# Kernel tuning notes

Measured on AMD Instinct MI355X. Metric: run time of the kernel, lower is better.

Reference implementation:

```python
import jax, jax.numpy as jnp
import numpy as np

N_NODES = 50000
N_EDGES = 800000
D_IN = 512
D_HID = 64
D_OUT = 40


def setup_inputs() -> dict:
    key = jax.random.key(0)
    ks = jax.random.split(key, 8)
    x = jax.random.normal(ks[0], (N_NODES, D_IN), dtype=jnp.float32)
    edge_index = jax.random.randint(ks[1], (2, N_EDGES), 0, N_NODES, dtype=jnp.int32)
    w_mul = jax.random.uniform(ks[2], (N_EDGES,), dtype=jnp.float32)
    s1 = 1.0 / np.sqrt(D_IN)
    s2 = 1.0 / np.sqrt(D_HID)
    W1 = jax.random.uniform(ks[3], (D_IN, D_HID), minval=-s1, maxval=s1, dtype=jnp.float32)
    b1 = jax.random.uniform(ks[4], (D_HID,), minval=-s1, maxval=s1, dtype=jnp.float32)
    W2 = jax.random.uniform(ks[5], (D_HID, D_OUT), minval=-s2, maxval=s2, dtype=jnp.float32)
    b2 = jax.random.uniform(ks[6], (D_OUT,), minval=-s2, maxval=s2, dtype=jnp.float32)
    return {"x": x, "edge_index": edge_index, "w_mul": w_mul,
            "W1": W1, "b1": b1, "W2": W2, "b2": b2}


def _conv(h, src, dst, w_mul, W, b, n_nodes):
    # linear transform, then gather-scale-scatter-add (PyG aggr='add')
    h = h @ W + b                      # [N, d_out]
    msg = w_mul[:, None] * h[src]      # [E, d_out] gather + scale
    return jax.ops.segment_sum(msg, dst, num_segments=n_nodes)  # scatter-add


def reference(x, edge_index, w_mul, W1, b1, W2, b2):
    n_nodes = x.shape[0]
    src, dst = edge_index[0], edge_index[1]  # flow: source_to_target
    h = _conv(x, src, dst, w_mul, W1, b1, n_nodes)
    h = jax.nn.relu(h)
    h = _conv(h, src, dst, w_mul, W2, b2, n_nodes)
    return jax.nn.log_softmax(h, axis=1)
```

## Files before the change

### kernel.cpp

```cpp
#include <hip/hip_runtime.h>
#include <math.h>

#define D_IN  512
#define D_HID 64
#define D_OUT 40
#define CAP   64

typedef __attribute__((ext_vector_type(8))) short bf16x8;
typedef __attribute__((ext_vector_type(4))) float f32x4;

static __device__ __forceinline__ unsigned short f2bf(float f) {
    unsigned u = __float_as_uint(f);
    return (unsigned short)((u + 0x7FFF + ((u >> 16) & 1)) >> 16);
}
static __device__ __forceinline__ float bf2f(unsigned short h) {
    return __uint_as_float(((unsigned)h) << 16);
}

__global__ __launch_bounds__(256)
void prep_all(int* __restrict__ cursor, const float* __restrict__ W1,
              unsigned short* __restrict__ w1T, const float* __restrict__ W2,
              unsigned short* __restrict__ w2T, int N) {
    const int i = blockIdx.x * blockDim.x + threadIdx.x;
    if (i < N) cursor[i] = 0;
    const int j = i - N;
    if (j >= 0 && j < D_IN * D_HID) {
        const int k = j >> 6, col = j & 63;
        w1T[col * D_IN + k] = f2bf(W1[j]);
    }
    const int l = j - D_IN * D_HID;
    if (l >= 0 && l < 48 * D_HID) {
        const int col = l >> 6, k = l & 63;
        w2T[l] = (col < D_OUT) ? f2bf(W2[k * D_OUT + col]) : 0;
    }
}

__global__ __launch_bounds__(256)
void scatter_cap(const int* __restrict__ src, const int* __restrict__ dstA,
                 const float* __restrict__ wm, int* __restrict__ cursor,
                 unsigned* __restrict__ edges, int E, int N) {
    const int slice = (N + 7) >> 3;
    const int lo = (blockIdx.x & 7) * slice;
    const int hi = min(N, lo + slice);
    const int nChunk = gridDim.x >> 3;
    const int per = (E + nChunk - 1) / nChunk;
    const int beg = (blockIdx.x >> 3) * per;
    const int end = min(E, beg + per);
    for (int e = beg + threadIdx.x; e < end; e += blockDim.x) {
        const int d = dstA[e];
        if (d >= lo && d < hi) {
            const int pos = atomicAdd(&cursor[d], 1);
            if (pos < CAP)
                edges[(size_t)d * CAP + pos] =
                    ((unsigned)src[e] << 16) | (unsigned)f2bf(wm[e]);
        }
    }
}

__global__ __launch_bounds__(256)
void gemm1_mfma(const float* __restrict__ x, const unsigned short* __restrict__ w1T,
                const float* __restrict__ b1, unsigned short* __restrict__ h1, int N) {
    __shared__ unsigned char lds[8192];
    const int t = threadIdx.x;
    const int lane = t & 63;
    const int wv = t >> 6;
    const int nodeBase = blockIdx.x * 64;
    const int fr = lane & 15;
    const int fc = lane >> 4;

    int gn = nodeBase + wv * 16 + fr; if (gn >= N) gn = N - 1;
    const float* xrow = x + (size_t)gn * D_IN + fc * 8;

    f32x4 acc[4];
#pragma unroll
    for (int cg = 0; cg < 4; ++cg) acc[cg] = (f32x4){0.f, 0.f, 0.f, 0.f};

    for (int k0 = 0; k0 < D_IN; k0 += 64) {
        __syncthreads();
#pragma unroll
        for (int hh = 0; hh < 2; ++hh) {
            const int g = t + hh * 256;
            const int col = g >> 3, slot = g & 7;
            const uint4 p = *reinterpret_cast<const uint4*>(
                w1T + (size_t)col * D_IN + k0 + slot * 8);
            *reinterpret_cast<uint4*>(
                lds + col * 128 + ((slot << 4) ^ ((col & 7) << 4))) = p;
        }
        __syncthreads();

#pragma unroll
        for (int s = 0; s < 2; ++s) {
            const float4 a = *reinterpret_cast<const float4*>(xrow + k0 + s * 32);
            const float4 b = *reinterpret_cast<const float4*>(xrow + k0 + s * 32 + 4);
            uint4 p;
            p.x = (unsigned)f2bf(a.x) | ((unsigned)f2bf(a.y) << 16);
            p.y = (unsigned)f2bf(a.z) | ((unsigned)f2bf(a.w) << 16);
            p.z = (unsigned)f2bf(b.x) | ((unsigned)f2bf(b.y) << 16);
            p.w = (unsigned)f2bf(b.z) | ((unsigned)f2bf(b.w) << 16);
            const bf16x8 afrag = *reinterpret_cast<const bf16x8*>(&p);
            const int slot = s * 4 + fc;
#pragma unroll
            for (int cg = 0; cg < 4; ++cg) {
                const int brow = cg * 16 + fr;
                const bf16x8 bfrag = *reinterpret_cast<const bf16x8*>(
                    lds + brow * 128 + ((slot << 4) ^ ((brow & 7) << 4)));
                acc[cg] = __builtin_amdgcn_mfma_f32_16x16x32_bf16(afrag, bfrag, acc[cg], 0, 0, 0);
            }
        }
    }

    const int rq = lane >> 4;
#pragma unroll
    for (int cg = 0; cg < 4; ++cg) {
        const int col = cg * 16 + fr;
        const float bb = b1[col];
#pragma unroll
        for (int r = 0; r < 4; ++r) {
            const int node = nodeBase + wv * 16 + rq * 4 + r;
            if (node < N)
                h1[(size_t)node * D_HID + col] = f2bf(acc[cg][r] + bb);
        }
    }
}

__global__ __launch_bounds__(256)
void agg_hid(const unsigned short* __restrict__ h, const unsigned* __restrict__ edges,
             const int* __restrict__ count, unsigned short* __restrict__ agg1, int N) {
    const int lane = threadIdx.x & 63;
    const int n = (blockIdx.x * blockDim.x + threadIdx.x) >> 6;
    if (n >= N) return;
    const unsigned er = edges[(size_t)n * CAP + lane];
    const int cnt = min(count[n], CAP);
    float acc = 0.f;
    int j = 0;
    for (; j + 8 <= cnt; j += 8) {
        unsigned p[8];
#pragma unroll
        for (int u = 0; u < 8; ++u) p[u] = (unsigned)__shfl((int)er, j + u);
        float v[8];
#pragma unroll
        for (int u = 0; u < 8; ++u) v[u] = bf2f(h[(size_t)(p[u] >> 16) * D_HID + lane]);
#pragma unroll
        for (int u = 0; u < 8; ++u)
            acc += bf2f((unsigned short)(p[u] & 0xffff)) * v[u];
    }
    for (; j < cnt; ++j) {
        const unsigned p0 = (unsigned)__shfl((int)er, j);
        acc += bf2f((unsigned short)(p0 & 0xffff)) *
               bf2f(h[(size_t)(p0 >> 16) * D_HID + lane]);
    }
    agg1[(size_t)n * D_HID + lane] = f2bf(fmaxf(acc, 0.f));
}

__global__ __launch_bounds__(256)
void gemm2_mfma(const unsigned short* __restrict__ agg1,
                const unsigned short* __restrict__ w2T,
                const float* __restrict__ b2, unsigned short* __restrict__ h2, int N) {
    __shared__ unsigned char lds[8192 + 6144];
    const int t = threadIdx.x;
    const int lane = t & 63;
    const int wv = t >> 6;
    const int nodeBase = blockIdx.x * 64;

#pragma unroll
    for (int hh = 0; hh < 2; ++hh) {
        const int g = t + hh * 256;
        const int row = g >> 3, slot = g & 7;
        int gn = nodeBase + row; if (gn >= N) gn = N - 1;
        const uint4 p = *reinterpret_cast<const uint4*>(agg1 + (size_t)gn * D_HID + slot * 8);
        *reinterpret_cast<uint4*>(lds + row * 128 + ((slot << 4) ^ ((row & 7) << 4))) = p;
    }
    for (int g = t; g < 384; g += 256) {
        const int row = g >> 3, slot = g & 7;
        const uint4 p = *reinterpret_cast<const uint4*>(w2T + (size_t)row * D_HID + slot * 8);
        *reinterpret_cast<uint4*>(lds + 8192 + row * 128 + ((slot << 4) ^ ((row & 7) << 4))) = p;
    }
    __syncthreads();

    f32x4 acc[3];
#pragma unroll
    for (int cg = 0; cg < 3; ++cg) acc[cg] = (f32x4){0.f, 0.f, 0.f, 0.f};

    const int fr = lane & 15;
    const int fc = lane >> 4;
#pragma unroll
    for (int s = 0; s < 2; ++s) {
        const int slot = s * 4 + fc;
        const int arow = wv * 16 + fr;
        const bf16x8 afrag = *reinterpret_cast<const bf16x8*>(
            lds + arow * 128 + ((slot << 4) ^ ((arow & 7) << 4)));
#pragma unroll
        for (int cg = 0; cg < 3; ++cg) {
            const int brow = cg * 16 + fr;
            const bf16x8 bfrag = *reinterpret_cast<const bf16x8*>(
                lds + 8192 + brow * 128 + ((slot << 4) ^ ((brow & 7) << 4)));
            acc[cg] = __builtin_amdgcn_mfma_f32_16x16x32_bf16(afrag, bfrag, acc[cg], 0, 0, 0);
        }
    }

    const int rq = lane >> 4;
#pragma unroll
    for (int cg = 0; cg < 3; ++cg) {
        const int col = cg * 16 + fr;
        if (col < D_OUT) {
            const float bb = b2[col];
#pragma unroll
            for (int r = 0; r < 4; ++r) {
                const int node = nodeBase + wv * 16 + rq * 4 + r;
                if (node < N)
                    h2[(size_t)node * D_OUT + col] = f2bf(acc[cg][r] + bb);
            }
        }
    }
}

__global__ __launch_bounds__(256)
void agg40_lsm(const unsigned short* __restrict__ h2, const unsigned* __restrict__ edges,
               const int* __restrict__ count, float* __restrict__ out, int N) {
    const int lane = threadIdx.x & 63;
    const int col  = (lane < D_OUT) ? lane : 0;
    const int n = (blockIdx.x * blockDim.x + threadIdx.x) >> 6;
    if (n >= N) return;
    const unsigned er = edges[(size_t)n * CAP + lane];
    const int cnt = min(count[n], CAP);
    float acc = 0.f;
    int j = 0;
    for (; j + 8 <= cnt; j += 8) {
        unsigned p[8];
#pragma unroll
        for (int u = 0; u < 8; ++u) p[u] = (unsigned)__shfl((int)er, j + u);
        float v[8];
#pragma unroll
        for (int u = 0; u < 8; ++u) v[u] = bf2f(h2[(size_t)(p[u] >> 16) * D_OUT + col]);
#pragma unroll
        for (int u = 0; u < 8; ++u)
            acc += bf2f((unsigned short)(p[u] & 0xffff)) * v[u];
    }
    for (; j < cnt; ++j) {
        const unsigned p0 = (unsigned)__shfl((int)er, j);
        acc += bf2f((unsigned short)(p0 & 0xffff)) *
               bf2f(h2[(size_t)(p0 >> 16) * D_OUT + col]);
    }
    const float v = (lane < D_OUT) ? acc : -INFINITY;
    float m = v;
#pragma unroll
    for (int o = 32; o > 0; o >>= 1) m = fmaxf(m, __shfl_xor(m, o, 64));
    float s = (lane < D_OUT) ? __expf(v - m) : 0.f;
#pragma unroll
    for (int o = 32; o > 0; o >>= 1) s += __shfl_xor(s, o, 64);
    if (lane < D_OUT) out[(size_t)n * D_OUT + lane] = v - m - __logf(s);
}

extern "C" void kernel_launch(void* const* d_in, const int* in_sizes, int n_in,
                              void* d_out, int out_size, void* d_ws, size_t ws_size,
                              hipStream_t stream) {
    const float* x   = (const float*)d_in[0];
    const int*   ei  = (const int*)d_in[1];
    const float* wm  = (const float*)d_in[2];
    const float* W1  = (const float*)d_in[3];
    const float* b1  = (const float*)d_in[4];
    const float* W2  = (const float*)d_in[5];
    const float* b2  = (const float*)d_in[6];

    const int N = in_sizes[0] / D_IN;
    const int E = in_sizes[2];
    const int* srcIdx = ei;
    const int* dstIdx = ei + E;

    unsigned short* w1T    = (unsigned short*)d_ws;
    unsigned short* h1bf   = w1T + (size_t)D_HID * D_IN;
    unsigned short* agg1bf = h1bf + (size_t)N * D_HID;
    unsigned* edges        = (unsigned*)(agg1bf + (size_t)N * D_HID);
    int*   cursor          = (int*)(edges + (size_t)N * CAP);
    unsigned short* w2T    = (unsigned short*)(cursor + N);
    unsigned short* h2bf   = h1bf;
    float* out             = (float*)d_out;

    const int prepWork = N + D_IN * D_HID + 48 * D_HID;

    prep_all<<<(prepWork + 255) / 256, 256, 0, stream>>>(cursor, W1, w1T, W2, w2T, N);
    scatter_cap<<<2048, 256, 0, stream>>>(srcIdx, dstIdx, wm, cursor, edges, E, N);
    gemm1_mfma<<<(N + 63) / 64, 256, 0, stream>>>(x, w1T, b1, h1bf, N);
    agg_hid<<<(N * 64 + 255) / 256, 256, 0, stream>>>(h1bf, edges, cursor, agg1bf, N);
    gemm2_mfma<<<(N + 63) / 64, 256, 0, stream>>>(agg1bf, w2T, b2, h2bf, N);
    agg40_lsm<<<(N * 64 + 255) / 256, 256, 0, stream>>>(h2bf, edges, cursor, out, N);
}
```

Measured before the change: 130.1 us.

## Fuse scatter with GEMM1 and aggregation with GEMM2 into two launches

Merges the edge-bucketing scatter and the first dense GEMM into one horizontally fused launch, using separate block ranges so the two independent jobs can overlap. It also fuses the hidden-layer aggregation into the second GEMM: each wave aggregates 16 nodes straight into LDS, prefetching the next node's edge row, so the agg1 round trip through global memory and two launches go away. The trade-off is that scatter blocks drop from 2048 to 1024. The fused B kernel also has one wave processing 16 nodes serially, which cuts the parallelism available to the latency-bound gather.

```diff
diff --git a/kernel.cpp b/kernel.cpp
--- a/kernel.cpp
+++ b/kernel.cpp
@@ -36,150 +36,154 @@
 }
 
 __global__ __launch_bounds__(256)
-void scatter_cap(const int* __restrict__ src, const int* __restrict__ dstA,
-                 const float* __restrict__ wm, int* __restrict__ cursor,
-                 unsigned* __restrict__ edges, int E, int N) {
-    const int slice = (N + 7) >> 3;
-    const int lo = (blockIdx.x & 7) * slice;
-    const int hi = min(N, lo + slice);
-    const int nChunk = gridDim.x >> 3;
-    const int per = (E + nChunk - 1) / nChunk;
-    const int beg = (blockIdx.x >> 3) * per;
-    const int end = min(E, beg + per);
-    for (int e = beg + threadIdx.x; e < end; e += blockDim.x) {
-        const int d = dstA[e];
-        if (d >= lo && d < hi) {
-            const int pos = atomicAdd(&cursor[d], 1);
-            if (pos < CAP)
-                edges[(size_t)d * CAP + pos] =
-                    ((unsigned)src[e] << 16) | (unsigned)f2bf(wm[e]);
-        }
-    }
-}
-
-__global__ __launch_bounds__(256)
-void gemm1_mfma(const float* __restrict__ x, const unsigned short* __restrict__ w1T,
-                const float* __restrict__ b1, unsigned short* __restrict__ h1, int N) {
+void fatA(const float* __restrict__ x, const unsigned short* __restrict__ w1T,
+          const float* __restrict__ b1, unsigned short* __restrict__ h1,
+          const int* __restrict__ src, const int* __restrict__ dstA,
+          const float* __restrict__ wm, int* __restrict__ cursor,
+          unsigned* __restrict__ edges, int E, int N, int g1Blocks) {
     __shared__ unsigned char lds[8192];
     const int t = threadIdx.x;
-    const int lane = t & 63;
-    const int wv = t >> 6;
-    const int nodeBase = blockIdx.x * 64;
-    const int fr = lane & 15;
-    const int fc = lane >> 4;
-
-    int gn = nodeBase + wv * 16 + fr; if (gn >= N) gn = N - 1;
-    const float* xrow = x + (size_t)gn * D_IN + fc * 8;
-
-    f32x4 acc[4];
-#pragma unroll
-    for (int cg = 0; cg < 4; ++cg) acc[cg] = (f32x4){0.f, 0.f, 0.f, 0.f};
-
-    for (int k0 = 0; k0 < D_IN; k0 += 64) {
-        __syncthreads();
-#pragma unroll
-        for (int hh = 0; hh < 2; ++hh) {
-            const int g = t + hh * 256;
-            const int col = g >> 3, slot = g & 7;
-            const uint4 p = *reinterpret_cast<const uint4*>(
-                w1T + (size_t)col * D_IN + k0 + slot * 8);
-            *reinterpret_cast<uint4*>(
-                lds + col * 128 + ((slot << 4) ^ ((col & 7) << 4))) = p;
-        }
-        __syncthreads();
-
-#pragma unroll
-        for (int s = 0; s < 2; ++s) {
-            const float4 a = *reinterpret_cast<const float4*>(xrow + k0 + s * 32);
-            const float4 b = *reinterpret_cast<const float4*>(xrow + k0 + s * 32 + 4);
-            uint4 p;
-            p.x = (unsigned)f2bf(a.x) | ((unsigned)f2bf(a.y) << 16);
-            p.y = (unsigned)f2bf(a.z) | ((unsigned)f2bf(a.w) << 16);
-            p.z = (unsigned)f2bf(b.x) | ((unsigned)f2bf(b.y) << 16);
-            p.w = (unsigned)f2bf(b.z) | ((unsigned)f2bf(b.w) << 16);
-            const bf16x8 afrag = *reinterpret_cast<const bf16x8*>(&p);
-            const int slot = s * 4 + fc;
-#pragma unroll
-            for (int cg = 0; cg < 4; ++cg) {
-                const int brow = cg * 16 + fr;
-                const bf16x8 bfrag = *reinterpret_cast<const bf16x8*>(
-                    lds + brow * 128 + ((slot << 4) ^ ((brow & 7) << 4)));
-                acc[cg] = __builtin_amdgcn_mfma_f32_16x16x32_bf16(afrag, bfrag, acc[cg], 0, 0, 0);
-            }
-        }
-    }
-
-    const int rq = lane >> 4;
-#pragma unroll
-    for (int cg = 0; cg < 4; ++cg) {
-        const int col = cg * 16 + fr;
-        const float bb = b1[col];
-#pragma unroll
-        for (int r = 0; r < 4; ++r) {
-            const int node = nodeBase + wv * 16 + rq * 4 + r;
-            if (node < N)
-                h1[(size_t)node * D_HID + col] = f2bf(acc[cg][r] + bb);
-        }
-    }
-}
-
-__global__ __launch_bounds__(256)
-void agg_hid(const unsigned short* __restrict__ h, const unsigned* __restrict__ edges,
-             const int* __restrict__ count, unsigned short* __restrict__ agg1, int N) {
-    const int lane = threadIdx.x & 63;
-    const int n = (blockIdx.x * blockDim.x + threadIdx.x) >> 6;
-    if (n >= N) return;
-    const unsigned er = edges[(size_t)n * CAP + lane];
-    const int cnt = min(count[n], CAP);
-    float acc = 0.f;
-    int j = 0;
-    for (; j + 8 <= cnt; j += 8) {
-        unsigned p[8];
-#pragma unroll
-        for (int u = 0; u < 8; ++u) p[u] = (unsigned)__shfl((int)er, j + u);
-        float v[8];
-#pragma unroll
-        for (int u = 0; u < 8; ++u) v[u] = bf2f(h[(size_t)(p[u] >> 16) * D_HID + lane]);
-#pragma unroll
-        for (int u = 0; u < 8; ++u)
-            acc += bf2f((unsigned short)(p[u] & 0xffff)) * v[u];
-    }
-    for (; j < cnt; ++j) {
-        const unsigned p0 = (unsigned)__shfl((int)er, j);
-        acc += bf2f((unsigned short)(p0 & 0xffff)) *
-               bf2f(h[(size_t)(p0 >> 16) * D_HID + lane]);
-    }
-    agg1[(size_t)n * D_HID + lane] = f2bf(fmaxf(acc, 0.f));
-}
-
-__global__ __launch_bounds__(256)
-void gemm2_mfma(const unsigned short* __restrict__ agg1,
-                const unsigned short* __restrict__ w2T,
-                const float* __restrict__ b2, unsigned short* __restrict__ h2, int N) {
+
+    if ((int)blockIdx.x < g1Blocks) {
+        const int lane = t & 63;
+        const int wv = t >> 6;
+        const int nodeBase = blockIdx.x * 64;
+        const int fr = lane & 15;
+        const int fc = lane >> 4;
+
+        int gn = nodeBase + wv * 16 + fr; if (gn >= N) gn = N - 1;
+        const float* xrow = x + (size_t)gn * D_IN + fc * 8;
+
+        f32x4 acc[4];
+#pragma unroll
+        for (int cg = 0; cg < 4; ++cg) acc[cg] = (f32x4){0.f, 0.f, 0.f, 0.f};
+
+        for (int k0 = 0; k0 < D_IN; k0 += 64) {
+            __syncthreads();
+#pragma unroll
+            for (int hh = 0; hh < 2; ++hh) {
+                const int g = t + hh * 256;
+                const int col = g >> 3, slot = g & 7;
+                const uint4 p = *reinterpret_cast<const uint4*>(
+                    w1T + (size_t)col * D_IN + k0 + slot * 8);
+                *reinterpret_cast<uint4*>(
+                    lds + col * 128 + ((slot << 4) ^ ((col & 7) << 4))) = p;
+            }
+            __syncthreads();
+
+#pragma unroll
+            for (int s = 0; s < 2; ++s) {
+                const float4 a = *reinterpret_cast<const float4*>(xrow + k0 + s * 32);
+                const float4 b = *reinterpret_cast<const float4*>(xrow + k0 + s * 32 + 4);
+                uint4 p;
+                p.x = (unsigned)f2bf(a.x) | ((unsigned)f2bf(a.y) << 16);
+                p.y = (unsigned)f2bf(a.z) | ((unsigned)f2bf(a.w) << 16);
+                p.z = (unsigned)f2bf(b.x) | ((unsigned)f2bf(b.y) << 16);
+                p.w = (unsigned)f2bf(b.z) | ((unsigned)f2bf(b.w) << 16);
+                const bf16x8 afrag = *reinterpret_cast<const bf16x8*>(&p);
+                const int slot = s * 4 + fc;
+#pragma unroll
+                for (int cg = 0; cg < 4; ++cg) {
+                    const int brow = cg * 16 + fr;
+                    const bf16x8 bfrag = *reinterpret_cast<const bf16x8*>(
+                        lds + brow * 128 + ((slot << 4) ^ ((brow & 7) << 4)));
+                    acc[cg] = __builtin_amdgcn_mfma_f32_16x16x32_bf16(afrag, bfrag, acc[cg], 0, 0, 0);
+                }
+            }
+        }
+
+        const int rq = lane >> 4;
+#pragma unroll
+        for (int cg = 0; cg < 4; ++cg) {
+            const int col = cg * 16 + fr;
+            const float bb = b1[col];
+#pragma unroll
+            for (int r = 0; r < 4; ++r) {
+                const int node = nodeBase + wv * 16 + rq * 4 + r;
+                if (node < N)
+                    h1[(size_t)node * D_HID + col] = f2bf(acc[cg][r] + bb);
+            }
+        }
+    } else {
+        const int slice = (N + 7) >> 3;
+        const int lo = (blockIdx.x & 7) * slice;
+        const int hi = min(N, lo + slice);
+        const int localBid = blockIdx.x - g1Blocks;
+        const int nChunk = (gridDim.x - g1Blocks) >> 3;
+        const int per = (E + nChunk - 1) / nChunk;
+        const int beg = (localBid >> 3) * per;
+        const int end = min(E, beg + per);
+        for (int e = beg + t; e < end; e += 256) {
+            const int d = dstA[e];
+            if (d >= lo && d < hi) {
+                const int pos = atomicAdd(&cursor[d], 1);
+                if (pos < CAP)
+                    edges[(size_t)d * CAP + pos] =
+                        ((unsigned)src[e] << 16) | (unsigned)f2bf(wm[e]);
+            }
+        }
+    }
+}
+
+__global__ __launch_bounds__(256)
+void fatB(const unsigned short* __restrict__ h1, const unsigned* __restrict__ edges,
+          const int* __restrict__ count, const unsigned short* __restrict__ w2T,
+          const float* __restrict__ b2, unsigned short* __restrict__ h2, int N) {
     __shared__ unsigned char lds[8192 + 6144];
     const int t = threadIdx.x;
     const int lane = t & 63;
     const int wv = t >> 6;
     const int nodeBase = blockIdx.x * 64;
 
-#pragma unroll
-    for (int hh = 0; hh < 2; ++hh) {
-        const int g = t + hh * 256;
-        const int row = g >> 3, slot = g & 7;
-        int gn = nodeBase + row; if (gn >= N) gn = N - 1;
-        const uint4 p = *reinterpret_cast<const uint4*>(agg1 + (size_t)gn * D_HID + slot * 8);
-        *reinterpret_cast<uint4*>(lds + row * 128 + ((slot << 4) ^ ((row & 7) << 4))) = p;
-    }
     for (int g = t; g < 384; g += 256) {
         const int row = g >> 3, slot = g & 7;
         const uint4 p = *reinterpret_cast<const uint4*>(w2T + (size_t)row * D_HID + slot * 8);
         *reinterpret_cast<uint4*>(lds + 8192 + row * 128 + ((slot << 4) ^ ((row & 7) << 4))) = p;
     }
+
+    {
+        const int n0 = nodeBase + wv * 16;
+        unsigned er = edges[(size_t)min(n0, N - 1) * CAP + lane];
+        int cnt = (n0 < N) ? min(count[n0], CAP) : 0;
+#pragma unroll 1
+        for (int i = 0; i < 16; ++i) {
+            const int r = wv * 16 + i;
+            unsigned erN = 0; int cntN = 0;
+            if (i < 15) {
+                const int nn = nodeBase + r + 1;
+                erN = edges[(size_t)min(nn, N - 1) * CAP + lane];
+                cntN = (nn < N) ? min(count[nn], CAP) : 0;
+            }
+            float acc = 0.f;
+            int j = 0;
+            for (; j + 8 <= cnt; j += 8) {
+                unsigned p[8];
+#pragma unroll
+                for (int u = 0; u < 8; ++u) p[u] = (unsigned)__shfl((int)er, j + u);
+                float v[8];
+#pragma unroll
+                for (int u = 0; u < 8; ++u)
+                    v[u] = bf2f(h1[(size_t)(p[u] >> 16) * D_HID + lane]);
+#pragma unroll
+                for (int u = 0; u < 8; ++u)
+                    acc += bf2f((unsigned short)(p[u] & 0xffff)) * v[u];
+            }
+            for (; j < cnt; ++j) {
+                const unsigned p0 = (unsigned)__shfl((int)er, j);
+                acc += bf2f((unsigned short)(p0 & 0xffff)) *
+                       bf2f(h1[(size_t)(p0 >> 16) * D_HID + lane]);
+            }
+            const unsigned short hv = f2bf(fmaxf(acc, 0.f));
+            *reinterpret_cast<unsigned short*>(
+                lds + r * 128 + (((lane >> 3) << 4) ^ ((r & 7) << 4)) + (lane & 7) * 2) = hv;
+            er = erN; cnt = cntN;
+        }
+    }
     __syncthreads();
 
-    f32x4 acc[3];
-#pragma unroll
-    for (int cg = 0; cg < 3; ++cg) acc[cg] = (f32x4){0.f, 0.f, 0.f, 0.f};
+    f32x4 acc2[3];
+#pragma unroll
+    for (int cg = 0; cg < 3; ++cg) acc2[cg] = (f32x4){0.f, 0.f, 0.f, 0.f};
 
     const int fr = lane & 15;
     const int fc = lane >> 4;
@@ -194,7 +198,7 @@
             const int brow = cg * 16 + fr;
             const bf16x8 bfrag = *reinterpret_cast<const bf16x8*>(
                 lds + 8192 + brow * 128 + ((slot << 4) ^ ((brow & 7) << 4)));
-            acc[cg] = __builtin_amdgcn_mfma_f32_16x16x32_bf16(afrag, bfrag, acc[cg], 0, 0, 0);
+            acc2[cg] = __builtin_amdgcn_mfma_f32_16x16x32_bf16(afrag, bfrag, acc2[cg], 0, 0, 0);
         }
     }
 
@@ -208,7 +212,7 @@
             for (int r = 0; r < 4; ++r) {
                 const int node = nodeBase + wv * 16 + rq * 4 + r;
                 if (node < N)
-                    h2[(size_t)node * D_OUT + col] = f2bf(acc[cg][r] + bb);
+                    h2[(size_t)node * D_OUT + col] = f2bf(acc2[cg][r] + bb);
             }
         }
     }
@@ -267,21 +271,21 @@
     const int* srcIdx = ei;
     const int* dstIdx = ei + E;
 
-    unsigned short* w1T    = (unsigned short*)d_ws;
-    unsigned short* h1bf   = w1T + (size_t)D_HID * D_IN;
-    unsigned short* agg1bf = h1bf + (size_t)N * D_HID;
-    unsigned* edges        = (unsigned*)(agg1bf + (size_t)N * D_HID);
-    int*   cursor          = (int*)(edges + (size_t)N * CAP);
-    unsigned short* w2T    = (unsigned short*)(cursor + N);
-    unsigned short* h2bf   = h1bf;
-    float* out             = (float*)d_out;
-
+    unsigned short* w1T  = (unsigned short*)d_ws;
+    unsigned short* h1bf = w1T + (size_t)D_HID * D_IN;
+    unsigned short* h2bf = h1bf + (size_t)N * D_HID;
+    unsigned* edges      = (unsigned*)(h2bf + (size_t)N * D_HID);
+    int*   cursor        = (int*)(edges + (size_t)N * CAP);
+    unsigned short* w2T  = (unsigned short*)(cursor + N);
+    float* out           = (float*)d_out;
+
+    const int g1Blocks = (N + 63) / 64;
+    const int scatterBlocks = 1024;
     const int prepWork = N + D_IN * D_HID + 48 * D_HID;
 
     prep_all<<<(prepWork + 255) / 256, 256, 0, stream>>>(cursor, W1, w1T, W2, w2T, N);
-    scatter_cap<<<2048, 256, 0, stream>>>(srcIdx, dstIdx, wm, cursor, edges, E, N);
-    gemm1_mfma<<<(N + 63) / 64, 256, 0, stream>>>(x, w1T, b1, h1bf, N);
-    agg_hid<<<(N * 64 + 255) / 256, 256, 0, stream>>>(h1bf, edges, cursor, agg1bf, N);
-    gemm2_mfma<<<(N + 63) / 64, 256, 0, stream>>>(agg1bf, w2T, b2, h2bf, N);
+    fatA<<<g1Blocks + scatterBlocks, 256, 0, stream>>>(
+        x, w1T, b1, h1bf, srcIdx, dstIdx, wm, cursor, edges, E, N, g1Blocks);
+    fatB<<<g1Blocks, 256, 0, stream>>>(h1bf, edges, cursor, w2T, b2, h2bf, N);
     agg40_lsm<<<(N * 64 + 255) / 256, 256, 0, stream>>>(h2bf, edges, cursor, out, N);
 }
```

Result: slower. 139.7 us (+7.4%).
